# Kernel tuning notes

Measured on AMD Instinct MI355X. Metric: run time of the kernel, lower is better.

## Reference

```python
import jax, jax.numpy as jnp
import numpy as np

HIDDEN = 2560
N_HEADS = 32
HEAD_DIM = HIDDEN // N_HEADS  # 80
ROPE_PCT = 0.25
ROT = int(HEAD_DIM * ROPE_PCT)  # 20
THETA = 10000.0


def setup_inputs() -> dict:
    key = jax.random.key(0)
    ks = jax.random.split(key, 6)
    B, S = 2, 2048
    hidden_states = jax.random.normal(ks[0], (B, S, HIDDEN), dtype=jnp.float32)
    attention_mask = jnp.ones((B, S), dtype=jnp.float32)  # unused in no-cache path
    position_ids = jnp.tile(jnp.arange(S, dtype=jnp.int32)[None, :], (B, 1))
    scale = 1.0 / np.sqrt(HIDDEN)
    Wq = jax.random.normal(ks[1], (HIDDEN, HIDDEN), dtype=jnp.float32) * scale
    Wk = jax.random.normal(ks[2], (HIDDEN, HIDDEN), dtype=jnp.float32) * scale
    Wv = jax.random.normal(ks[3], (HIDDEN, HIDDEN), dtype=jnp.float32) * scale
    Wo = jax.random.normal(ks[4], (HIDDEN, HIDDEN), dtype=jnp.float32) * scale
    return {"hidden_states": hidden_states, "attention_mask": attention_mask,
            "position_ids": position_ids, "Wq": Wq, "Wk": Wk, "Wv": Wv, "Wo": Wo}


def _rotate_half(x):
    x1, x2 = jnp.split(x, 2, axis=-1)
    return jnp.concatenate([-x2, x1], axis=-1)


def _rope_cos_sin(position_ids, dtype):
    # inv_freq over rotary dims
    inv_freq = 1.0 / (THETA ** (jnp.arange(0, ROT, 2, dtype=jnp.float32) / ROT))
    pos = position_ids.astype(jnp.float32)  # [B,S]
    freqs = pos[..., None] * inv_freq[None, None, :]  # [B,S,ROT/2]
    emb = jnp.concatenate([freqs, freqs], axis=-1)    # [B,S,ROT]
    cos = jnp.cos(emb)[:, None, :, :].astype(dtype)   # [B,1,S,ROT]
    sin = jnp.sin(emb)[:, None, :, :].astype(dtype)
    return cos, sin


def reference(hidden_states, attention_mask, position_ids, Wq, Wk, Wv, Wo):
    B, S, H = hidden_states.shape
    dtype = hidden_states.dtype
    # projections: [B,S,H] -> [B,nh,S,hd]
    def split_heads(x):
        return x.reshape(B, S, N_HEADS, HEAD_DIM).transpose(0, 2, 1, 3)
    q = split_heads(hidden_states @ Wq)
    k = split_heads(hidden_states @ Wk)
    v = split_heads(hidden_states @ Wv)

    # partial RoPE on first ROT dims
    cos, sin = _rope_cos_sin(position_ids, dtype)
    q_rot, q_pass = q[..., :ROT], q[..., ROT:]
    k_rot, k_pass = k[..., :ROT], k[..., ROT:]
    q_rot = q_rot * cos + _rotate_half(q_rot) * sin
    k_rot = k_rot * cos + _rotate_half(k_rot) * sin
    q = jnp.concatenate([q_rot, q_pass], axis=-1)
    k = jnp.concatenate([k_rot, k_pass], axis=-1)

    # causal attention (no KV cache -> is_causal=True SDPA path)
    scale = 1.0 / np.sqrt(HEAD_DIM)
    scores = jnp.einsum("bhqd,bhkd->bhqk", q, k) * scale
    causal = jnp.tril(jnp.ones((S, S), dtype=bool))
    scores = jnp.where(causal[None, None, :, :], scores, jnp.finfo(jnp.float32).min)
    probs = jax.nn.softmax(scores.astype(jnp.float32), axis=-1).astype(dtype)
    attn = jnp.einsum("bhqk,bhkd->bhqd", probs, v)
    attn = attn.transpose(0, 2, 1, 3).reshape(B, S, H)
    return attn @ Wo
```

## Files before the change

### kernel.cpp

```cpp
#include <hip/hip_runtime.h>
#include <stdint.h>

typedef unsigned short u16;
typedef __bf16 bf16x8 __attribute__((ext_vector_type(8)));
typedef float floatx4 __attribute__((ext_vector_type(4)));

#define HIDDEN 2560
#define NHEADS 32
#define HD 80
#define SEQ 2048
#define BATCH 2
#define MROWS (BATCH*SEQ)
#define QB 128

__device__ __forceinline__ float bf2f(uint32_t bits) {
    return __uint_as_float(bits << 16);
}
__device__ __forceinline__ u16 f2bf_bits(float f) {
    uint32_t x = __float_as_uint(f);
    uint32_t r = (x + 0x7fffu + ((x >> 16) & 1u)) >> 16;
    return (u16)r;
}
__device__ __forceinline__ floatx4 mk4(float x) {
    return (floatx4){x, x, x, x};
}
__device__ __forceinline__ floatx4 max4(floatx4 a, floatx4 b) {
    floatx4 r;
#pragma unroll
    for (int i = 0; i < 4; i++) r[i] = fmaxf(a[i], b[i]);
    return r;
}
__device__ __forceinline__ floatx4 exp4(floatx4 a) {
    floatx4 r;
#pragma unroll
    for (int i = 0; i < 4; i++) r[i] = __expf(a[i]);
    return r;
}
__device__ __forceinline__ floatx4 shfl_xor4(floatx4 v, int mask) {
    floatx4 r;
#pragma unroll
    for (int i = 0; i < 4; i++) r[i] = __shfl_xor(v[i], mask, 64);
    return r;
}
__device__ __forceinline__ void gload16(const u16* g, u16* l) {
    __builtin_amdgcn_global_load_lds(
        (const __attribute__((address_space(1))) uint32_t*)g,
        (__attribute__((address_space(3))) uint32_t*)l, 16, 0, 0);
}

__global__ __launch_bounds__(256) void split_x(const float* __restrict__ in,
                                               u16* __restrict__ hi,
                                               u16* __restrict__ lo) {
    size_t i4 = (size_t)blockIdx.x * 256 + threadIdx.x;
    float4 v = ((const float4*)in)[i4];
    float f[4] = {v.x, v.y, v.z, v.w};
    u16 h[4], l[4];
#pragma unroll
    for (int j = 0; j < 4; j++) {
        h[j] = f2bf_bits(f[j]);
        l[j] = f2bf_bits(f[j] - bf2f(h[j]));
    }
    ((uint2*)hi)[i4] = *(uint2*)h;
    ((uint2*)lo)[i4] = *(uint2*)l;
}

__global__ __launch_bounds__(256) void split_wt(const float* __restrict__ in,
                                                u16* __restrict__ outh,
                                                u16* __restrict__ outl) {
    __shared__ float t[64][65];
    int k0 = blockIdx.x * 64;
    int n0 = blockIdx.y * 64;
    int tid = threadIdx.x;
    int rr = tid >> 4;
    int c4 = (tid & 15) * 4;
#pragma unroll
    for (int it = 0; it < 4; it++) {
        int row = it * 16 + rr;
        float4 v = *(const float4*)&in[(size_t)(k0 + row) * HIDDEN + n0 + c4];
        t[row][c4 + 0] = v.x; t[row][c4 + 1] = v.y;
        t[row][c4 + 2] = v.z; t[row][c4 + 3] = v.w;
    }
    __syncthreads();
#pragma unroll
    for (int it = 0; it < 4; it++) {
        int row = it * 16 + rr;
        float f[4] = { t[c4 + 0][row], t[c4 + 1][row], t[c4 + 2][row], t[c4 + 3][row] };
        u16 h[4], l[4];
#pragma unroll
        for (int j = 0; j < 4; j++) {
            h[j] = f2bf_bits(f[j]);
            l[j] = f2bf_bits(f[j] - bf2f(h[j]));
        }
        size_t o = (size_t)(n0 + row) * HIDDEN + k0 + c4;
        *(uint2*)&outh[o] = *(uint2*)h;
        *(uint2*)&outl[o] = *(uint2*)l;
    }
}

__global__ __launch_bounds__(256) void gemm_bt2(const u16* __restrict__ Ah,
                                                const u16* __restrict__ Al,
                                                const u16* __restrict__ Bh,
                                                const u16* __restrict__ Bl,
                                                float* __restrict__ C) {
    __shared__ u16 lAh[128 * 32];
    __shared__ u16 lAl[128 * 32];
    __shared__ u16 lBh[128 * 32];
    __shared__ u16 lBl[128 * 32];
    const int K = HIDDEN;
    int tid  = threadIdx.x;
    int lane = tid & 63;
    int wave = tid >> 6;
    int wr = wave >> 1, wc = wave & 1;
    int m0 = blockIdx.y * 128, n0 = blockIdx.x * 128;
    int lr = lane & 15, lq = lane >> 4;

    int srow = wave * 32 + (lane >> 2);
    int scol = ((lane & 3) ^ ((lane >> 3) & 3)) * 8;
    const u16* gAh = Ah + (size_t)(m0 + srow) * K + scol;
    const u16* gAl = Al + (size_t)(m0 + srow) * K + scol;
    const u16* gBh = Bh + (size_t)(n0 + srow) * K + scol;
    const u16* gBl = Bl + (size_t)(n0 + srow) * K + scol;
    const size_t q1 = (size_t)16 * K;
    u16* dAh = &lAh[(wave * 32) * 32];
    u16* dAl = &lAl[(wave * 32) * 32];
    u16* dBh = &lBh[(wave * 32) * 32];
    u16* dBl = &lBl[(wave * 32) * 32];

    floatx4 acc[4][4];
#pragma unroll
    for (int i = 0; i < 4; i++)
#pragma unroll
        for (int j = 0; j < 4; j++)
            acc[i][j] = mk4(0.f);

    int swz = (lr >> 1) & 3;
    int rsl = (lq ^ swz) * 8;

    for (int k0 = 0; k0 < K; k0 += 32) {
        gload16(gAh + k0, dAh);  gload16(gAh + q1 + k0, dAh + 16 * 32);
        gload16(gAl + k0, dAl);  gload16(gAl + q1 + k0, dAl + 16 * 32);
        gload16(gBh + k0, dBh);  gload16(gBh + q1 + k0, dBh + 16 * 32);
        gload16(gBl + k0, dBl);  gload16(gBl + q1 + k0, dBl + 16 * 32);
        __syncthreads();
        bf16x8 ah[4], al[4], bh[4], bl[4];
#pragma unroll
        for (int i = 0; i < 4; i++) {
            int ra = (wr * 64 + i * 16 + lr) * 32 + rsl;
            int rb = (wc * 64 + i * 16 + lr) * 32 + rsl;
            ah[i] = *(const bf16x8*)&lAh[ra];
            al[i] = *(const bf16x8*)&lAl[ra];
            bh[i] = *(const bf16x8*)&lBh[rb];
            bl[i] = *(const bf16x8*)&lBl[rb];
        }
#pragma unroll
        for (int i = 0; i < 4; i++)
#pragma unroll
            for (int j = 0; j < 4; j++) {
                acc[i][j] = __builtin_amdgcn_mfma_f32_16x16x32_bf16(ah[i], bh[j], acc[i][j], 0, 0, 0);
                acc[i][j] = __builtin_amdgcn_mfma_f32_16x16x32_bf16(ah[i], bl[j], acc[i][j], 0, 0, 0);
                acc[i][j] = __builtin_amdgcn_mfma_f32_16x16x32_bf16(al[i], bh[j], acc[i][j], 0, 0, 0);
            }
        __syncthreads();
    }
#pragma unroll
    for (int i = 0; i < 4; i++) {
        int rowb = m0 + wr * 64 + i * 16 + lq * 4;
#pragma unroll
        for (int j = 0; j < 4; j++) {
            int col = n0 + wc * 64 + j * 16 + lr;
#pragma unroll
            for (int r = 0; r < 4; r++)
                C[(size_t)(rowb + r) * HIDDEN + col] = acc[i][j][r];
        }
    }
}

__global__ __launch_bounds__(256) void rope_k(float* __restrict__ Qb, float* __restrict__ Kb,
                                              const int* __restrict__ pos_ids) {
    int idx = blockIdx.x * 256 + threadIdx.x;
    int row = idx >> 5;
    int h   = idx & 31;
    float pos = (float)pos_ids[row];
    size_t base = (size_t)row * HIDDEN + h * HD;
    float* q = Qb + base;
    float* k = Kb + base;
#pragma unroll
    for (int i = 0; i < 10; i++) {
        float freq = pos * exp2f(-1.3287712379549449f * (float)i);
        float sn, cs;
        sincosf(freq, &sn, &cs);
        float q1 = q[i], q2 = q[i + 10];
        q[i]      = q1 * cs - q2 * sn;
        q[i + 10] = q2 * cs + q1 * sn;
        float k1 = k[i], k2 = k[i + 10];
        k[i]      = k1 * cs - k2 * sn;
        k[i + 10] = k2 * cs + k1 * sn;
    }
}

__global__ __launch_bounds__(256) void vtrans(const float* __restrict__ Vb,
                                              u16* __restrict__ Vth,
                                              u16* __restrict__ Vtl) {
    __shared__ float t[64][81];
    int bh = blockIdx.x; int b = bh >> 5, h = bh & 31;
    int s0 = blockIdx.y * 64;
    int tid = threadIdx.x;
    for (int idx = tid; idx < 64 * 20; idx += 256) {
        int s = idx / 20, c = idx % 20;
        float4 v = *(const float4*)&Vb[(size_t)(b * SEQ + s0 + s) * HIDDEN + h * HD + c * 4];
        t[s][c * 4 + 0] = v.x; t[s][c * 4 + 1] = v.y;
        t[s][c * 4 + 2] = v.z; t[s][c * 4 + 3] = v.w;
    }
    __syncthreads();
    for (int idx = tid; idx < 80 * 8; idx += 256) {
        int d = idx >> 3, sc = idx & 7;
        u16 hh[8], ll[8];
#pragma unroll
        for (int j = 0; j < 8; j++) {
            float f = t[sc * 8 + j][d];
            hh[j] = f2bf_bits(f);
            ll[j] = f2bf_bits(f - bf2f(hh[j]));
        }
        size_t o = ((size_t)bh * HD + d) * SEQ + s0 + sc * 8;
        *(int4*)&Vth[o] = *(int4*)hh;
        *(int4*)&Vtl[o] = *(int4*)ll;
    }
}

__global__ __launch_bounds__(256) void attn_mfma(const u16* __restrict__ Qh_,
                                                 const u16* __restrict__ Ql_,
                                                 const u16* __restrict__ Kh_,
                                                 const u16* __restrict__ Kl_,
                                                 const u16* __restrict__ Vth_,
                                                 const u16* __restrict__ Vtl_,
                                                 u16* __restrict__ Oh_,
                                                 u16* __restrict__ Ol_) {
    __shared__ u16 lds[15616];
    u16* lKh = lds;
    u16* lKl = lds + 3328;
    u16* lVh = lds + 6656;
    u16* lVl = lds + 9856;
    u16* lP  = lds + 13056;

    int tid = threadIdx.x;
    int lane = tid & 63, w = tid >> 6;
    int lr = lane & 15, lq = lane >> 4;
    int bh = blockIdx.x; int b = bh >> 5, h = bh & 31;
    int qblk = (gridDim.y - 1) - blockIdx.y;
    int q0 = qblk * QB;
    size_t rowbase = (size_t)b * SEQ;
    size_t hoff = (size_t)h * HD;
    const float SC = 0.11180339887498949f;

    bf16x8 qh[2][3], ql[2][3];
#pragma unroll
    for (int round = 0; round < 2; round++) {
        for (int idx = tid; idx < 1280; idx += 256) {
            int buf = idx >= 640; int e = idx - buf * 640;
            int r = e / 10, c = e % 10;
            const u16* src = (buf ? Ql_ : Qh_) +
                (rowbase + q0 + round * 64 + r) * HIDDEN + hoff + c * 8;
            *(int4*)&lds[buf * 6656 + r * 104 + c * 8] = *(const int4*)src;
        }
        {
            int idx = tid;
            if (idx < 256) {
                int buf = idx >= 128; int e = idx - buf * 128;
                int r = e >> 1, hf = e & 1;
                *(int4*)&lds[buf * 6656 + r * 104 + 80 + hf * 8] = make_int4(0, 0, 0, 0);
            }
        }
        __syncthreads();
        if ((w >> 1) == round) {
            int wl = w & 1;
#pragma unroll
            for (int rt = 0; rt < 2; rt++) {
                int lrow = wl * 32 + rt * 16 + lr;
#pragma unroll
                for (int c = 0; c < 3; c++) {
                    qh[rt][c] = *(const bf16x8*)&lds[lrow * 104 + c * 32 + lq * 8];
                    ql[rt][c] = *(const bf16x8*)&lds[6656 + lrow * 104 + c * 32 + lq * 8];
                }
            }
        }
        __syncthreads();
    }
    if (tid < 128) {
        int buf = tid >= 64; int e = tid - buf * 64;
        int r = e >> 1, hf = e & 1;
        *(int4*)&lds[buf * 3328 + r * 104 + 80 + hf * 8] = make_int4(0, 0, 0, 0);
    }

    floatx4 acc[2][5];
    floatx4 mrow[2], lsum[2];
#pragma unroll
    for (int rt = 0; rt < 2; rt++) {
        mrow[rt] = mk4(-3.0e38f);
        lsum[rt] = mk4(0.f);
#pragma unroll
        for (int nt = 0; nt < 5; nt++) acc[rt][nt] = mk4(0.f);
    }

    int ntiles = 4 * qblk + 4;
    int qw0 = q0 + w * 32;
    u16* lPw = lP + w * 640;

    for (int t = 0; t < ntiles; t++) {
        int k0 = t * 32;
        for (int idx = tid; idx < 1280; idx += 256) {
            if (idx < 640) {
                int buf = idx >= 320; int e = idx - buf * 320;
                int r = e / 10, c = e % 10;
                const u16* src = (buf ? Kl_ : Kh_) +
                    (rowbase + k0 + r) * HIDDEN + hoff + c * 8;
                *(int4*)&lds[buf * 3328 + r * 104 + c * 8] = *(const int4*)src;
            } else {
                int e2 = idx - 640;
                int buf = e2 >= 320; int e = e2 - buf * 320;
                int d = e >> 2, kc = e & 3;
                const u16* src = (buf ? Vtl_ : Vth_) +
                    ((size_t)bh * HD + d) * SEQ + k0 + kc * 8;
                *(int4*)&lds[6656 + buf * 3200 + d * 40 + kc * 8] = *(const int4*)src;
            }
        }
        __syncthreads();
        if (k0 <= qw0 + 31) {
#pragma unroll
            for (int rt = 0; rt < 2; rt++) {
                int qrt0 = qw0 + rt * 16;
                if (k0 > qrt0 + 15) continue;
                floatx4 s[2];
#pragma unroll
                for (int st = 0; st < 2; st++) {
                    floatx4 sv = mk4(0.f);
#pragma unroll
                    for (int c = 0; c < 3; c++) {
                        bf16x8 kh = *(const bf16x8*)&lKh[(st * 16 + lr) * 104 + c * 32 + lq * 8];
                        bf16x8 kl = *(const bf16x8*)&lKl[(st * 16 + lr) * 104 + c * 32 + lq * 8];
                        sv = __builtin_amdgcn_mfma_f32_16x16x32_bf16(qh[rt][c], kh, sv, 0, 0, 0);
                        sv = __builtin_amdgcn_mfma_f32_16x16x32_bf16(qh[rt][c], kl, sv, 0, 0, 0);
                        sv = __builtin_amdgcn_mfma_f32_16x16x32_bf16(ql[rt][c], kh, sv, 0, 0, 0);
                    }
                    s[st] = sv;
                }
                int qg0 = qrt0 + lq * 4;
                int c0 = k0 + lr, c1 = c0 + 16;
#pragma unroll
                for (int r = 0; r < 4; r++) {
                    s[0][r] = (c0 <= qg0 + r) ? s[0][r] * SC : -3.0e38f;
                    s[1][r] = (c1 <= qg0 + r) ? s[1][r] * SC : -3.0e38f;
                }
                floatx4 rm = max4(s[0], s[1]);
#pragma unroll
                for (int off = 1; off < 16; off <<= 1) rm = max4(rm, shfl_xor4(rm, off));
                floatx4 mnew = max4(mrow[rt], rm);
                floatx4 alpha = exp4(mrow[rt] - mnew);
                mrow[rt] = mnew;
                floatx4 p0 = exp4(s[0] - mnew);
                floatx4 p1 = exp4(s[1] - mnew);
                floatx4 rs = p0 + p1;
#pragma unroll
                for (int off = 1; off < 16; off <<= 1) rs = rs + shfl_xor4(rs, off);
                lsum[rt] = lsum[rt] * alpha + rs;
#pragma unroll
                for (int nt = 0; nt < 5; nt++) acc[rt][nt] *= alpha;
#pragma unroll
                for (int r = 0; r < 4; r++) {
                    lPw[(lq * 4 + r) * 40 + lr]      = f2bf_bits(p0[r]);
                    lPw[(lq * 4 + r) * 40 + 16 + lr] = f2bf_bits(p1[r]);
                }
                __builtin_amdgcn_s_waitcnt(0xC07F);
                bf16x8 pa = *(const bf16x8*)&lPw[lr * 40 + lq * 8];
#pragma unroll
                for (int nt = 0; nt < 5; nt++) {
                    bf16x8 vh = *(const bf16x8*)&lVh[(nt * 16 + lr) * 40 + lq * 8];
                    bf16x8 vl = *(const bf16x8*)&lVl[(nt * 16 + lr) * 40 + lq * 8];
                    acc[rt][nt] = __builtin_amdgcn_mfma_f32_16x16x32_bf16(pa, vh, acc[rt][nt], 0, 0, 0);
                    acc[rt][nt] = __builtin_amdgcn_mfma_f32_16x16x32_bf16(pa, vl, acc[rt][nt], 0, 0, 0);
                }
            }
        }
        __syncthreads();
    }
#pragma unroll
    for (int rt = 0; rt < 2; rt++) {
        floatx4 inv;
#pragma unroll
        for (int r = 0; r < 4; r++) inv[r] = 1.f / lsum[rt][r];
#pragma unroll
        for (int nt = 0; nt < 5; nt++) {
#pragma unroll
            for (int r = 0; r < 4; r++) {
                float o = acc[rt][nt][r] * inv[r];
                u16 hh = f2bf_bits(o);
                u16 ll = f2bf_bits(o - bf2f(hh));
                size_t row = rowbase + qw0 + rt * 16 + lq * 4 + r;
                Oh_[row * HIDDEN + hoff + nt * 16 + lr] = hh;
                Ol_[row * HIDDEN + hoff + nt * 16 + lr] = ll;
            }
        }
    }
}

extern "C" void kernel_launch(void* const* d_in, const int* in_sizes, int n_in,
                              void* d_out, int out_size, void* d_ws, size_t ws_size,
                              hipStream_t stream) {
    const float* hidden = (const float*)d_in[0];
    const int* pos    = (const int*)d_in[2];
    const float* Wq   = (const float*)d_in[3];
    const float* Wk   = (const float*)d_in[4];
    const float* Wv   = (const float*)d_in[5];
    const float* Wo   = (const float*)d_in[6];

    const size_t NQ = (size_t)MROWS * HIDDEN;
    float* ws = (float*)d_ws;
    float* Qb = ws;
    float* Kb = ws + NQ;
    float* Vb = ws + 2 * NQ;
    u16* Ah  = (u16*)(ws + 3 * NQ);
    u16* Al  = Ah + NQ;
    u16* WTh = Al + NQ;
    u16* WTl = WTh + (size_t)HIDDEN * HIDDEN;
    u16* Vth = Ah;
    u16* Vtl = Al;
    u16* Qh  = (u16*)Vb;
    u16* Ql  = Qh + NQ;
    u16* Kh  = (u16*)Qb;
    u16* Kl  = Kh + NQ;
    u16* Oh  = (u16*)Kb;
    u16* Ol  = Oh + NQ;

    dim3 blk(256);
    dim3 wgrid(HIDDEN / 64, HIDDEN / 64);
    dim3 ggrid(HIDDEN / 128, MROWS / 128);

    split_x<<<dim3(NQ / 1024), blk, 0, stream>>>(hidden, Ah, Al);
    split_wt<<<wgrid, blk, 0, stream>>>(Wq, WTh, WTl);
    gemm_bt2<<<ggrid, blk, 0, stream>>>(Ah, Al, WTh, WTl, Qb);
    split_wt<<<wgrid, blk, 0, stream>>>(Wk, WTh, WTl);
    gemm_bt2<<<ggrid, blk, 0, stream>>>(Ah, Al, WTh, WTl, Kb);
    split_wt<<<wgrid, blk, 0, stream>>>(Wv, WTh, WTl);
    gemm_bt2<<<ggrid, blk, 0, stream>>>(Ah, Al, WTh, WTl, Vb);
    rope_k<<<dim3(MROWS * NHEADS / 256), blk, 0, stream>>>(Qb, Kb, pos);
    vtrans<<<dim3(BATCH * NHEADS, SEQ / 64), blk, 0, stream>>>(Vb, Vth, Vtl);
    split_x<<<dim3(NQ / 1024), blk, 0, stream>>>(Qb, Qh, Ql);
    split_x<<<dim3(NQ / 1024), blk, 0, stream>>>(Kb, Kh, Kl);
    attn_mfma<<<dim3(BATCH * NHEADS, SEQ / QB), blk, 0, stream>>>(Qh, Ql, Kh, Kl,
                                                                  Vth, Vtl, Oh, Ol);
    split_wt<<<wgrid, blk, 0, stream>>>(Wo, WTh, WTl);
    gemm_bt2<<<ggrid, blk, 0, stream>>>(Oh, Ol, WTh, WTl, (float*)d_out);
}
```

Measured before the change: 1.345 ms.

## Double-buffer K/V via async LDS loads, trim QK MFMAs, lazy softmax rescale

Replaces the synchronous register-staged K/V tile loads with global_load_lds into a double-buffered, XOR-swizzled LDS layout, so the next tile is prefetched while the current one computes. The last 16 head dims are handled with a cheaper 2-MFMA tail instead of a zero-padded third chunk (8 instead of 9 MFMAs per score tile). Row reductions use DPP row rotates instead of shuffles, and the softmax skips rescaling acc and the running max while the new max stays within 8 of the old one. It also adds s_setprio around compute. The cost is doubled LDS use and a wave-uniform branch, and the lazy max bounds each exponent by e^8, which is safe in fp32.

New measurement: 1.330 ms. No clear change (-1.1%).

```diff
diff --git a/kernel.cpp b/kernel.cpp
--- a/kernel.cpp
+++ b/kernel.cpp
@@ -36,11 +36,28 @@
     for (int i = 0; i < 4; i++) r[i] = __expf(a[i]);
     return r;
 }
-__device__ __forceinline__ floatx4 shfl_xor4(floatx4 v, int mask) {
+template <int N>
+__device__ __forceinline__ floatx4 ror16_4(floatx4 v) {
     floatx4 r;
 #pragma unroll
-    for (int i = 0; i < 4; i++) r[i] = __shfl_xor(v[i], mask, 64);
+    for (int i = 0; i < 4; i++)
+        r[i] = __int_as_float(__builtin_amdgcn_update_dpp(
+            0, __float_as_int(v[i]), 0x120 + N, 0xF, 0xF, true));
     return r;
+}
+__device__ __forceinline__ floatx4 redmax16(floatx4 v) {
+    v = max4(v, ror16_4<1>(v));
+    v = max4(v, ror16_4<2>(v));
+    v = max4(v, ror16_4<4>(v));
+    v = max4(v, ror16_4<8>(v));
+    return v;
+}
+__device__ __forceinline__ floatx4 redsum16(floatx4 v) {
+    v = v + ror16_4<1>(v);
+    v = v + ror16_4<2>(v);
+    v = v + ror16_4<4>(v);
+    v = v + ror16_4<8>(v);
+    return v;
 }
 __device__ __forceinline__ void gload16(const u16* g, u16* l) {
     __builtin_amdgcn_global_load_lds(
@@ -235,12 +252,7 @@
                                                  const u16* __restrict__ Vtl_,
                                                  u16* __restrict__ Oh_,
                                                  u16* __restrict__ Ol_) {
-    __shared__ u16 lds[15616];
-    u16* lKh = lds;
-    u16* lKl = lds + 3328;
-    u16* lVh = lds + 6656;
-    u16* lVl = lds + 9856;
-    u16* lP  = lds + 13056;
+    __shared__ u16 lds[22784];
 
     int tid = threadIdx.x;
     int lane = tid & 63, w = tid >> 6;
@@ -252,7 +264,7 @@
     size_t hoff = (size_t)h * HD;
     const float SC = 0.11180339887498949f;
 
-    bf16x8 qh[2][3], ql[2][3];
+    bf16x8 qh[2][2], ql[2][2], qta[2], qtb[2];
 #pragma unroll
     for (int round = 0; round < 2; round++) {
         for (int idx = tid; idx < 1280; idx += 256) {
@@ -262,33 +274,25 @@
                 (rowbase + q0 + round * 64 + r) * HIDDEN + hoff + c * 8;
             *(int4*)&lds[buf * 6656 + r * 104 + c * 8] = *(const int4*)src;
         }
-        {
-            int idx = tid;
-            if (idx < 256) {
-                int buf = idx >= 128; int e = idx - buf * 128;
-                int r = e >> 1, hf = e & 1;
-                *(int4*)&lds[buf * 6656 + r * 104 + 80 + hf * 8] = make_int4(0, 0, 0, 0);
-            }
-        }
         __syncthreads();
         if ((w >> 1) == round) {
             int wl = w & 1;
+            int tba = (lq >> 1) ? 6656 : 0;
+            int tbb = (lq >> 1) ? 0 : 6656;
+            int tcol = 64 + (lq & 1) * 8;
 #pragma unroll
             for (int rt = 0; rt < 2; rt++) {
                 int lrow = wl * 32 + rt * 16 + lr;
 #pragma unroll
-                for (int c = 0; c < 3; c++) {
+                for (int c = 0; c < 2; c++) {
                     qh[rt][c] = *(const bf16x8*)&lds[lrow * 104 + c * 32 + lq * 8];
                     ql[rt][c] = *(const bf16x8*)&lds[6656 + lrow * 104 + c * 32 + lq * 8];
                 }
+                qta[rt] = *(const bf16x8*)&lds[tba + lrow * 104 + tcol];
+                qtb[rt] = *(const bf16x8*)&lds[tbb + lrow * 104 + tcol];
             }
         }
         __syncthreads();
-    }
-    if (tid < 128) {
-        int buf = tid >= 64; int e = tid - buf * 64;
-        int r = e >> 1, hf = e & 1;
-        *(int4*)&lds[buf * 3328 + r * 104 + 80 + hf * 8] = make_int4(0, 0, 0, 0);
     }
 
     floatx4 acc[2][5];
@@ -303,28 +307,62 @@
 
     int ntiles = 4 * qblk + 4;
     int qw0 = q0 + w * 32;
-    u16* lPw = lP + w * 640;
+    u16* lPw = lds + 20480 + w * 576;
+
+    int k0RowOff = (lane >> 3) * HIDDEN + (((lane & 7) ^ (lane >> 3)) * 8);
+    int k1RowOff = (lane >> 1) * HIDDEN + 64 + (lane & 1) * 8;
+    int vRowOff  = (lane >> 2) * SEQ + ((((lane & 3) ^ ((lane >> 3) & 3))) * 8);
+    const u16* kSrc = (w & 1 ? Kl_ : Kh_) + rowbase * HIDDEN + hoff;
+    const u16* vSrc = (w == 3 ? Vtl_ : Vth_) + (size_t)bh * HD * SEQ;
+
+    auto stage = [&](int t, int bsel) {
+        int k0 = t * 32;
+        u16* B = lds + bsel * 10240;
+        if (w < 2) {
+            const u16* kb = kSrc + (size_t)k0 * HIDDEN;
+            u16* d0 = B + w * 2048;
+#pragma unroll
+            for (int j = 0; j < 4; j++)
+                gload16(kb + (size_t)j * 8 * HIDDEN + k0RowOff, d0 + j * 512);
+            gload16(kb + k1RowOff, B + 4096 + w * 512);
+        } else {
+            const u16* vb = vSrc + k0;
+            u16* d0 = B + 5120 + (w == 3 ? 2560 : 0);
+#pragma unroll
+            for (int j = 0; j < 5; j++)
+                gload16(vb + (size_t)j * 16 * SEQ + vRowOff, d0 + j * 512);
+        }
+    };
+
+    int ks0 = ((lq) ^ (lr & 7)) * 8;
+    int ks1 = ((4 + lq) ^ (lr & 7)) * 8;
+    int k1off = (lq >> 1) * 512 + (lq & 1) * 8;
+    int vsl = (lq ^ ((lr >> 1) & 3)) * 8;
+
+    stage(0, 0);
 
     for (int t = 0; t < ntiles; t++) {
         int k0 = t * 32;
-        for (int idx = tid; idx < 1280; idx += 256) {
-            if (idx < 640) {
-                int buf = idx >= 320; int e = idx - buf * 320;
-                int r = e / 10, c = e % 10;
-                const u16* src = (buf ? Kl_ : Kh_) +
-                    (rowbase + k0 + r) * HIDDEN + hoff + c * 8;
-                *(int4*)&lds[buf * 3328 + r * 104 + c * 8] = *(const int4*)src;
-            } else {
-                int e2 = idx - 640;
-                int buf = e2 >= 320; int e = e2 - buf * 320;
-                int d = e >> 2, kc = e & 3;
-                const u16* src = (buf ? Vtl_ : Vth_) +
-                    ((size_t)bh * HD + d) * SEQ + k0 + kc * 8;
-                *(int4*)&lds[6656 + buf * 3200 + d * 40 + kc * 8] = *(const int4*)src;
+        __syncthreads();
+        if (t + 1 < ntiles) stage(t + 1, (t + 1) & 1);
+        u16* B = lds + (t & 1) * 10240;
+        if (k0 <= qw0 + 31) {
+            u16* bK0h = B;
+            u16* bK0l = B + 2048;
+            u16* bK1  = B + 4096;
+            u16* bVh  = B + 5120;
+            u16* bVl  = B + 7680;
+            __builtin_amdgcn_s_setprio(1);
+            bf16x8 kfh[2][2], kfl[2][2], k1f[2];
+#pragma unroll
+            for (int st = 0; st < 2; st++) {
+                int krow = st * 16 + lr;
+                kfh[st][0] = *(const bf16x8*)&bK0h[krow * 64 + ks0];
+                kfh[st][1] = *(const bf16x8*)&bK0h[krow * 64 + ks1];
+                kfl[st][0] = *(const bf16x8*)&bK0l[krow * 64 + ks0];
+                kfl[st][1] = *(const bf16x8*)&bK0l[krow * 64 + ks1];
+                k1f[st] = *(const bf16x8*)&bK1[krow * 16 + k1off];
             }
-        }
-        __syncthreads();
-        if (k0 <= qw0 + 31) {
 #pragma unroll
             for (int rt = 0; rt < 2; rt++) {
                 int qrt0 = qw0 + rt * 16;
@@ -333,14 +371,14 @@
 #pragma unroll
                 for (int st = 0; st < 2; st++) {
                     floatx4 sv = mk4(0.f);
-#pragma unroll
-                    for (int c = 0; c < 3; c++) {
-                        bf16x8 kh = *(const bf16x8*)&lKh[(st * 16 + lr) * 104 + c * 32 + lq * 8];
-                        bf16x8 kl = *(const bf16x8*)&lKl[(st * 16 + lr) * 104 + c * 32 + lq * 8];
-                        sv = __builtin_amdgcn_mfma_f32_16x16x32_bf16(qh[rt][c], kh, sv, 0, 0, 0);
-                        sv = __builtin_amdgcn_mfma_f32_16x16x32_bf16(qh[rt][c], kl, sv, 0, 0, 0);
-                        sv = __builtin_amdgcn_mfma_f32_16x16x32_bf16(ql[rt][c], kh, sv, 0, 0, 0);
-                    }
+                    sv = __builtin_amdgcn_mfma_f32_16x16x32_bf16(qh[rt][0], kfh[st][0], sv, 0, 0, 0);
+                    sv = __builtin_amdgcn_mfma_f32_16x16x32_bf16(qh[rt][0], kfl[st][0], sv, 0, 0, 0);
+                    sv = __builtin_amdgcn_mfma_f32_16x16x32_bf16(ql[rt][0], kfh[st][0], sv, 0, 0, 0);
+                    sv = __builtin_amdgcn_mfma_f32_16x16x32_bf16(qh[rt][1], kfh[st][1], sv, 0, 0, 0);
+                    sv = __builtin_amdgcn_mfma_f32_16x16x32_bf16(qh[rt][1], kfl[st][1], sv, 0, 0, 0);
+                    sv = __builtin_amdgcn_mfma_f32_16x16x32_bf16(ql[rt][1], kfh[st][1], sv, 0, 0, 0);
+                    sv = __builtin_amdgcn_mfma_f32_16x16x32_bf16(qta[rt], k1f[st], sv, 0, 0, 0);
+                    sv = __builtin_amdgcn_mfma_f32_16x16x32_bf16(qtb[rt], k1f[st], sv, 0, 0, 0);
                     s[st] = sv;
                 }
                 int qg0 = qrt0 + lq * 4;
@@ -350,37 +388,41 @@
                     s[0][r] = (c0 <= qg0 + r) ? s[0][r] * SC : -3.0e38f;
                     s[1][r] = (c1 <= qg0 + r) ? s[1][r] * SC : -3.0e38f;
                 }
-                floatx4 rm = max4(s[0], s[1]);
-#pragma unroll
-                for (int off = 1; off < 16; off <<= 1) rm = max4(rm, shfl_xor4(rm, off));
-                floatx4 mnew = max4(mrow[rt], rm);
-                floatx4 alpha = exp4(mrow[rt] - mnew);
-                mrow[rt] = mnew;
-                floatx4 p0 = exp4(s[0] - mnew);
-                floatx4 p1 = exp4(s[1] - mnew);
-                floatx4 rs = p0 + p1;
-#pragma unroll
-                for (int off = 1; off < 16; off <<= 1) rs = rs + shfl_xor4(rs, off);
-                lsum[rt] = lsum[rt] * alpha + rs;
-#pragma unroll
-                for (int nt = 0; nt < 5; nt++) acc[rt][nt] *= alpha;
+                floatx4 rm = redmax16(max4(s[0], s[1]));
+                int small = (rm[0] <= mrow[rt][0] + 8.f) & (rm[1] <= mrow[rt][1] + 8.f) &
+                            (rm[2] <= mrow[rt][2] + 8.f) & (rm[3] <= mrow[rt][3] + 8.f);
+                floatx4 p0, p1;
+                if (__all(small)) {
+                    p0 = exp4(s[0] - mrow[rt]);
+                    p1 = exp4(s[1] - mrow[rt]);
+                    lsum[rt] = lsum[rt] + redsum16(p0 + p1);
+                } else {
+                    floatx4 mnew = max4(mrow[rt], rm);
+                    floatx4 alpha = exp4(mrow[rt] - mnew);
+                    mrow[rt] = mnew;
+                    p0 = exp4(s[0] - mnew);
+                    p1 = exp4(s[1] - mnew);
+                    lsum[rt] = lsum[rt] * alpha + redsum16(p0 + p1);
+#pragma unroll
+                    for (int nt = 0; nt < 5; nt++) acc[rt][nt] *= alpha;
+                }
 #pragma unroll
                 for (int r = 0; r < 4; r++) {
-                    lPw[(lq * 4 + r) * 40 + lr]      = f2bf_bits(p0[r]);
-                    lPw[(lq * 4 + r) * 40 + 16 + lr] = f2bf_bits(p1[r]);
+                    lPw[(lq * 4 + r) * 36 + lr]      = f2bf_bits(p0[r]);
+                    lPw[(lq * 4 + r) * 36 + 16 + lr] = f2bf_bits(p1[r]);
                 }
                 __builtin_amdgcn_s_waitcnt(0xC07F);
-                bf16x8 pa = *(const bf16x8*)&lPw[lr * 40 + lq * 8];
+                bf16x8 pa = *(const bf16x8*)&lPw[lr * 36 + lq * 8];
 #pragma unroll
                 for (int nt = 0; nt < 5; nt++) {
-                    bf16x8 vh = *(const bf16x8*)&lVh[(nt * 16 + lr) * 40 + lq * 8];
-                    bf16x8 vl = *(const bf16x8*)&lVl[(nt * 16 + lr) * 40 + lq * 8];
+                    bf16x8 vh = *(const bf16x8*)&bVh[(nt * 16 + lr) * 32 + vsl];
+                    bf16x8 vl = *(const bf16x8*)&bVl[(nt * 16 + lr) * 32 + vsl];
                     acc[rt][nt] = __builtin_amdgcn_mfma_f32_16x16x32_bf16(pa, vh, acc[rt][nt], 0, 0, 0);
                     acc[rt][nt] = __builtin_amdgcn_mfma_f32_16x16x32_bf16(pa, vl, acc[rt][nt], 0, 0, 0);
                 }
             }
-        }
-        __syncthreads();
+            __builtin_amdgcn_s_setprio(0);
+        }
     }
 #pragma unroll
     for (int rt = 0; rt < 2; rt++) {
```
